# Kernel optimization log

Measured on AMD Instinct MI355X. Metric: run time of the kernel, lower is better.

## Reference

```python
import jax, jax.numpy as jnp
import numpy as np

N = 50000      # nodes
E = 800000     # edges (avg degree 16)
F = 6          # input node features
C = 64         # conv_hidden_channels
M = 256        # mlp_hidden_channels
NCLS = 24      # num_classes
EPS = 1e-5     # BatchNorm eps


def _bn(h, g, b):
    # BatchNorm1d in training mode: biased batch stats over the batch axis
    mu = h.mean(axis=0)
    var = ((h - mu) ** 2).mean(axis=0)
    return g * (h - mu) * jax.lax.rsqrt(var + EPS) + b


def _block(x, W, b, g, beta):
    # Lin -> ReLU -> BN  (one MLP block)
    return _bn(jax.nn.relu(x @ W + b), g, beta)


def _edge_conv(x, src, dst, Wa, ba, ga, bea, Wb, bb, gb, beb):
    # EdgeConv: message = MLP([x_i, x_j - x_i]), max-aggregated onto target i
    xi = x[dst]                                   # [E, d]
    xj = x[src]                                   # [E, d]
    e = jnp.concatenate([xi, xj - xi], axis=-1)   # [E, 2d]
    h = _block(_block(e, Wa, ba, ga, bea), Wb, bb, gb, beb)  # [E, C]
    agg = jax.ops.segment_max(h, dst, num_segments=N)        # [N, C]
    return jnp.where(jnp.isfinite(agg), agg, 0.0)  # zero-fill isolated nodes


def setup_inputs() -> dict:
    key = jax.random.key(0)
    ks = jax.random.split(key, 12)

    def w(k, shape, fan_in):
        return jax.random.normal(k, shape, jnp.float32) * (1.0 / np.sqrt(fan_in))

    z = lambda *s: jnp.zeros(s, jnp.float32)
    o = lambda *s: jnp.ones(s, jnp.float32)

    x = jax.random.normal(ks[0], (N, F), jnp.float32)
    edge_index = jax.random.randint(ks[1], (2, E), 0, N, jnp.int32)

    return {
        "x": x,
        # conv1 MLP: Lin(2F,C)+BN, Lin(C,C)+BN
        "W1a": w(ks[2], (2 * F, C), 2 * F), "b1a": z(C), "g1a": o(C), "be1a": z(C),
        "W1b": w(ks[3], (C, C), C),         "b1b": z(C), "g1b": o(C), "be1b": z(C),
        # conv2/conv3 stacked: Lin(2C,C)+BN, Lin(C,C)+BN
        "Wa": w(ks[4], (2, 2 * C, C), 2 * C), "ba": z(2, C), "ga": o(2, C), "bea": z(2, C),
        "Wb": w(ks[5], (2, C, C), C),         "bb": z(2, C), "gb": o(2, C), "beb": z(2, C),
        # lin1: Lin(3C, M)+BN
        "Wl": w(ks[6], (3 * C, M), 3 * C), "bl": z(M), "gl": o(M), "bel": z(M),
        # head: Lin(M, M/4)+BN, Lin(M/4, M/8)+BN, Lin(M/8, NCLS)
        "Wm1": w(ks[7], (M, M // 4), M),      "bm1": z(M // 4), "gm1": o(M // 4), "bem1": z(M // 4),
        "Wm2": w(ks[8], (M // 4, M // 8), M // 4), "bm2": z(M // 8), "gm2": o(M // 8), "bem2": z(M // 8),
        "Wo": w(ks[9], (M // 8, NCLS), M // 8), "bo": z(NCLS),
        "edge_index": edge_index,
    }


def reference(x, W1a, b1a, g1a, be1a, W1b, b1b, g1b, be1b,
              Wa, ba, ga, bea, Wb, bb, gb, beb,
              Wl, bl, gl, bel,
              Wm1, bm1, gm1, bem1, Wm2, bm2, gm2, bem2,
              Wo, bo, edge_index):
    src, dst = edge_index[0], edge_index[1]
    x1 = _edge_conv(x,  src, dst, W1a, b1a, g1a, be1a, W1b, b1b, g1b, be1b)
    x2 = _edge_conv(x1, src, dst, Wa[0], ba[0], ga[0], bea[0], Wb[0], bb[0], gb[0], beb[0])
    x3 = _edge_conv(x2, src, dst, Wa[1], ba[1], ga[1], bea[1], Wb[1], bb[1], gb[1], beb[1])
    h = _block(jnp.concatenate([x1, x2, x3], axis=-1), Wl, bl, gl, bel)
    h = _block(h, Wm1, bm1, gm1, bem1)   # Dropout is identity (eval)
    h = _block(h, Wm2, bm2, gm2, bem2)   # Dropout is identity (eval)
    logits = h @ Wo + bo
    return jax.nn.log_softmax(logits, axis=1)
```

## Files before the change

kernel.cpp:

```cpp
#include <hip/hip_runtime.h>
#include <hip/hip_bf16.h>

#define EPS 1e-5f
typedef unsigned short bfr;
typedef unsigned short hfr;
typedef _Float16 h2v __attribute__((ext_vector_type(2)));
typedef _Float16 f16x8 __attribute__((ext_vector_type(8)));
typedef float f32x4 __attribute__((ext_vector_type(4)));

#if defined(__has_builtin)
#if __has_builtin(__builtin_amdgcn_fdot2)
#define HAS_FDOT2 1
#endif
#endif

static inline int cdiv(int a, int b){ return (a + b - 1) / b; }
static inline int imin(int a, int b){ return a < b ? a : b; }

__device__ __forceinline__ float bf2f(bfr u){ return __uint_as_float((unsigned)u << 16); }
__device__ __forceinline__ bfr f2bf(float f){
  unsigned u = __float_as_uint(f);
  u += 0x7fffu + ((u >> 16) & 1u);
  return (bfr)(u >> 16);
}
__device__ __forceinline__ unsigned pack2bf(float a, float b){
  return (unsigned)f2bf(a) | ((unsigned)f2bf(b) << 16);
}
__device__ __forceinline__ float h2f(hfr u){ _Float16 h; __builtin_memcpy(&h, &u, 2); return (float)h; }
__device__ __forceinline__ hfr f2h(float f){ _Float16 h = (_Float16)f; hfr u; __builtin_memcpy(&u, &h, 2); return u; }
__device__ __forceinline__ unsigned pack2h(float a, float b){
  return (unsigned)f2h(a) | ((unsigned)f2h(b) << 16);
}
__device__ __forceinline__ h2v u2h2(unsigned u){ h2v r; __builtin_memcpy(&r, &u, 4); return r; }
__device__ __forceinline__ unsigned h22u(h2v h){ unsigned u; __builtin_memcpy(&u, &h, 4); return u; }
__device__ __forceinline__ float dot2(h2v a, h2v b, float c){
#ifdef HAS_FDOT2
  return __builtin_amdgcn_fdot2(a, b, c, false);
#else
  return c + (float)a.x * (float)b.x + (float)a.y * (float)b.y;
#endif
}

__global__ __launch_bounds__(256) void detect_kernel(const bfr* __restrict__ xr, int nwords, int* __restrict__ flag){
  int i = threadIdx.x;
  int bad = 0;
  if (i < nwords){
    bfr lo = xr[2 * i];
    int e = (lo >> 7) & 0xFF;
    bool plausible = ((lo & 0x7FFF) == 0) || (e >= 97 && e <= 157);
    bad = plausible ? 0 : 1;
  }
  __shared__ int s[256];
  s[threadIdx.x] = bad; __syncthreads();
  for (int st = 128; st; st >>= 1){
    if (threadIdx.x < st) s[threadIdx.x] += s[threadIdx.x + st];
    __syncthreads();
  }
  if (threadIdx.x == 0) *flag = (s[0] > 32) ? 1 : 0;
}

#define NPAR 31
struct ParamPtrs { const void* p[NPAR]; };
struct ParamOfs  { int off[NPAR + 1]; };

__global__ __launch_bounds__(256) void acvt_batch_kernel(ParamPtrs pp, ParamOfs po,
                                                         float* __restrict__ out, int total,
                                                         const int* __restrict__ flag){
  int g = blockIdx.x * 256 + threadIdx.x;
  if (g >= total) return;
  int isf = *flag;
  int t = 0;
  while (po.off[t + 1] <= g) ++t;
  int i = g - po.off[t];
  out[g] = isf ? ((const float*)pp.p[t])[i] : bf2f(((const bfr*)pp.p[t])[i]);
}

__global__ __launch_bounds__(256) void deg_kernel(const int* __restrict__ dst, int* __restrict__ deg, int E){
  int e = blockIdx.x * 256 + threadIdx.x;
  if (e < E) atomicAdd(&deg[dst[e]], 1);
}

__global__ __launch_bounds__(256) void scan1_kernel(const int* __restrict__ deg, int* __restrict__ locoff,
                                                    int* __restrict__ bsum, int N){
  __shared__ int s[256];
  int i = blockIdx.x * 256 + threadIdx.x;
  int v = (i < N) ? deg[i] : 0;
  s[threadIdx.x] = v; __syncthreads();
  for (int st = 1; st < 256; st <<= 1){
    int u = (threadIdx.x >= st) ? s[threadIdx.x - st] : 0;
    __syncthreads();
    s[threadIdx.x] += u;
    __syncthreads();
  }
  if (i < N) locoff[i] = s[threadIdx.x] - v;
  if (threadIdx.x == 255) bsum[blockIdx.x] = s[255];
}

__global__ __launch_bounds__(256) void scan2_kernel(int* __restrict__ bsum, int nb){
  __shared__ int s[256];
  const int t = threadIdx.x;
  int carry = 0;
  for (int base = 0; base < nb; base += 256){
    int v = (base + t < nb) ? bsum[base + t] : 0;
    s[t] = v; __syncthreads();
    for (int st = 1; st < 256; st <<= 1){
      int u = (t >= st) ? s[t - st] : 0;
      __syncthreads();
      s[t] += u;
      __syncthreads();
    }
    if (base + t < nb) bsum[base + t] = carry + s[t] - v;
    carry += s[255];
    __syncthreads();
  }
}

__global__ __launch_bounds__(256) void scan3_kernel(const int* __restrict__ locoff, const int* __restrict__ bsum,
                                                    int* __restrict__ row_off, int* __restrict__ cur,
                                                    int N, int E){
  int i = blockIdx.x * 256 + threadIdx.x;
  if (i < N){
    int v = locoff[i] + bsum[blockIdx.x];
    row_off[i] = v; cur[i] = v;
  }
  if (i == 0) row_off[N] = E;
}

__global__ __launch_bounds__(256) void scatter_kernel(const int* __restrict__ src, const int* __restrict__ dst,
                                                      int* __restrict__ cur, int* __restrict__ ssrc,
                                                      int* __restrict__ sdst, int E){
  int e = blockIdx.x * 256 + threadIdx.x;
  if (e < E){
    int d = dst[e];
    int p = atomicAdd(&cur[d], 1);
    ssrc[p] = src[e];
    sdst[p] = d;
  }
}

template<bool FIRST>
__global__ __launch_bounds__(256) void gemmPQ_kernel(const void* __restrict__ Av, int lda,
                                                     const float* __restrict__ Wa, int d,
                                                     const float* __restrict__ ba,
                                                     hfr* __restrict__ P, hfr* __restrict__ Q, int N){
  __shared__ unsigned WsU[64 * 64];
  const int y = blockIdx.y;
  const int tot = d * 64;
  if (FIRST){
    float* Ws = (float*)WsU;
    for (int i = threadIdx.x; i < tot; i += 256)
      Ws[i] = y ? Wa[tot + i] : (Wa[i] - Wa[tot + i]);
  } else {
    for (int i = threadIdx.x; i < 32 * 64; i += 256){
      int p = i >> 6, c = i & 63;
      int i0 = (2 * p) * 64 + c, i1 = (2 * p + 1) * 64 + c;
      float w0 = y ? Wa[tot + i0] : (Wa[i0] - Wa[tot + i0]);
      float w1 = y ? Wa[tot + i1] : (Wa[i1] - Wa[tot + i1]);
      WsU[i] = pack2h(w0, w1);
    }
  }
  __syncthreads();
  const int row = blockIdx.x * 256 + threadIdx.x;
  if (row >= N) return;
  float acc[64];
#pragma unroll
  for (int c = 0; c < 64; ++c) acc[c] = 0.f;
  if (FIRST){
    const float* Ws = (const float*)WsU;
    const float* Af = (const float*)Av + (size_t)row * lda;
    for (int k = 0; k < d; ++k){
      float a = Af[k];
      const float* wr = Ws + k * 64;
#pragma unroll
      for (int c4 = 0; c4 < 16; ++c4){
        float4 w = *(const float4*)(wr + 4 * c4);
        acc[4*c4+0] += a * w.x; acc[4*c4+1] += a * w.y;
        acc[4*c4+2] += a * w.z; acc[4*c4+3] += a * w.w;
      }
    }
  } else {
    const hfr* Ah = (const hfr*)Av + (size_t)row * lda;
#pragma unroll
    for (int k8 = 0; k8 < 8; ++k8){
      uint4 av = *(const uint4*)(Ah + k8 * 8);
      unsigned pr[4] = {av.x, av.y, av.z, av.w};
#pragma unroll
      for (int pi = 0; pi < 4; ++pi){
        h2v ap = u2h2(pr[pi]);
        const unsigned* wr = WsU + (k8 * 4 + pi) * 64;
#pragma unroll
        for (int c = 0; c < 64; ++c) acc[c] = dot2(ap, u2h2(wr[c]), acc[c]);
      }
    }
  }
  if (!y){
#pragma unroll
    for (int c = 0; c < 64; ++c) acc[c] += ba[c];
  }
  unsigned p[32];
#pragma unroll
  for (int c = 0; c < 64; c += 2) p[c / 2] = pack2h(acc[c], acc[c + 1]);
  hfr* outp = (y ? Q : P) + (size_t)row * 64;
  uint4* op = (uint4*)outp;
#pragma unroll
  for (int i = 0; i < 8; ++i) op[i] = make_uint4(p[4*i], p[4*i+1], p[4*i+2], p[4*i+3]);
}

template<int NOUT, int KSTEPS, bool FOLD>
__global__ __launch_bounds__(256) void mgemm_kernel(const hfr* __restrict__ Ah, int lda,
                                                    const float* __restrict__ Wp, const float* __restrict__ Wm, int ldw,
                                                    const float* __restrict__ bias,
                                                    const float* __restrict__ stats, float cntInv,
                                                    const float* __restrict__ g, const float* __restrict__ be,
                                                    hfr* __restrict__ Ov, int ldo,
                                                    int nrows, int relu){
  constexpr int K  = KSTEPS * 32;
  constexpr int KP = K + 8;
  constexpr int NT = NOUT / 16;
  __shared__ __align__(16) _Float16 W2T[NOUT * KP];
  __shared__ __align__(16) _Float16 etile[4][16][NOUT + 8];
  __shared__ float aS[FOLD ? K : 1], bbS[FOLD ? K : 1], bsum[FOLD ? 256 : 1];
  __shared__ float bfull[NOUT];
  const int tid = threadIdx.x;
  const int lane = tid & 63;
  const int wib = tid >> 6;
  const int colbase = blockIdx.y * NOUT;

  if (FOLD){
    for (int k = tid; k < K; k += 256){
      float mu = stats[k] * cntInv;
      float var = stats[K + k] * cntInv - mu * mu;
      float ai = g[k] * rsqrtf(var + EPS);
      aS[k] = ai; bbS[k] = be[k] - ai * mu;
    }
    __syncthreads();
  }
  for (int i = tid; i < K * NOUT; i += 256){
    int k = i / NOUT, c = i - k * NOUT;
    float w = Wp[(size_t)k * ldw + colbase + c];
    if (Wm) w -= Wm[(size_t)k * ldw + colbase + c];
    if (FOLD) w *= aS[k];
    W2T[c * KP + k] = (_Float16)w;
  }
  if (FOLD){
    constexpr int parts = 256 / NOUT;
    int c = tid % NOUT, p = tid / NOUT;
    float s = 0.f;
    for (int k = p; k < K; k += parts) s += bbS[k] * Wp[(size_t)k * ldw + colbase + c];
    bsum[p * NOUT + c] = s;
    __syncthreads();
    if (tid < NOUT){
      float t = bias[colbase + tid];
#pragma unroll
      for (int pp = 0; pp < parts; ++pp) t += bsum[pp * NOUT + tid];
      bfull[tid] = t;
    }
  } else {
    if (tid < NOUT) bfull[tid] = bias ? bias[colbase + tid] : 0.f;
  }
  __syncthreads();

  f16x8 Bf[KSTEPS][NT];
#pragma unroll
  for (int s = 0; s < KSTEPS; ++s)
#pragma unroll
    for (int t = 0; t < NT; ++t)
      Bf[s][t] = *(const f16x8*)&W2T[(t * 16 + (lane & 15)) * KP + s * 32 + (lane >> 4) * 8];
  float bc[NT];
#pragma unroll
  for (int t = 0; t < NT; ++t) bc[t] = bfull[t * 16 + (lane & 15)];

  const int ntiles = (nrows + 63) >> 6;
  for (int tile = blockIdx.x; tile < ntiles; tile += gridDim.x){
    const int r0 = tile * 64 + wib * 16;
    const int rowA = min(r0 + (lane & 15), nrows - 1);
    const hfr* Ap = Ah + (size_t)rowA * lda + (lane >> 4) * 8;
    f32x4 acc[NT];
#pragma unroll
    for (int t = 0; t < NT; ++t) acc[t] = (f32x4){bc[t], bc[t], bc[t], bc[t]};
#pragma unroll
    for (int s = 0; s < KSTEPS; ++s){
      f16x8 Af = *(const f16x8*)(Ap + s * 32);
#pragma unroll
      for (int t = 0; t < NT; ++t)
        acc[t] = __builtin_amdgcn_mfma_f32_16x16x32_f16(Af, Bf[s][t], acc[t], 0, 0, 0);
    }
#pragma unroll
    for (int t = 0; t < NT; ++t){
#pragma unroll
      for (int r = 0; r < 4; ++r){
        float v = acc[t][r];
        v = relu ? fmaxf(v, 0.f) : v;
        etile[wib][(lane >> 4) * 4 + r][t * 16 + (lane & 15)] = (_Float16)v;
      }
    }
    if (NOUT == 64){
#pragma unroll
      for (int h = 0; h < 2; ++h){
        int rl = h * 8 + (lane >> 3);
        int ch = lane & 7;
        uint4 vv = *(const uint4*)&etile[wib][rl][ch * 8];
        int rg = r0 + rl;
        if (rg < nrows) *(uint4*)(Ov + (size_t)rg * ldo + colbase + ch * 8) = vv;
      }
    } else {
      int rl = lane >> 2;
      int ch = lane & 3;
      uint4 vv = *(const uint4*)&etile[wib][rl][ch * 8];
      int rg = r0 + rl;
      if (rg < nrows) *(uint4*)(Ov + (size_t)rg * ldo + colbase + ch * 8) = vv;
    }
  }
}

__global__ __launch_bounds__(256) void passA_kernel(const hfr* __restrict__ P, const hfr* __restrict__ Q,
                                                    const int* __restrict__ ssrc, const int* __restrict__ sdst,
                                                    float* __restrict__ stats, int E){
  const int tid = threadIdx.x;
  const int lane = tid & 63;
  const int wib = tid >> 6;
  const int er0 = lane >> 3;
  const int ck = lane & 7;
  const int wid = (blockIdx.x * 256 + tid) >> 6;
  const int nw = (gridDim.x * 256) >> 6;
  const _Float16 z16 = (_Float16)0;
  const int lim = E - 1;
  float s8[8], q8[8];
#pragma unroll
  for (int j = 0; j < 8; ++j){ s8[j] = 0.f; q8[j] = 0.f; }
  for (int base = wid * 16; base < E; base += nw * 16){
    int idx = min(base + (lane & 15), lim);
    int sv = ssrc[idx];
    int dv = sdst[idx];
#pragma unroll
    for (int h = 0; h < 2; ++h){
      int er = h * 8 + er0;
      bool valid = (base + er) < E;
      int sj = __shfl(sv, er, 64);
      int dj = __shfl(dv, er, 64);
      uint4 qv = *((const uint4*)(Q + (size_t)sj * 64) + ck);
      uint4 pv = *((const uint4*)(P + (size_t)dj * 64) + ck);
      unsigned qa[4] = {qv.x, qv.y, qv.z, qv.w};
      unsigned pa[4] = {pv.x, pv.y, pv.z, pv.w};
#pragma unroll
      for (int t = 0; t < 4; ++t){
        h2v sm = u2h2(qa[t]) + u2h2(pa[t]);
        float v0 = (sm.x < z16) ? 0.f : (float)sm.x;
        float v1 = (sm.y < z16) ? 0.f : (float)sm.y;
        v0 = valid ? v0 : 0.f; v1 = valid ? v1 : 0.f;
        s8[2*t]   += v0; q8[2*t]   += v0 * v0;
        s8[2*t+1] += v1; q8[2*t+1] += v1 * v1;
      }
    }
  }
#pragma unroll
  for (int j = 0; j < 8; ++j){
    float s = s8[j], q = q8[j];
    s += __shfl_xor(s, 8, 64);  q += __shfl_xor(q, 8, 64);
    s += __shfl_xor(s, 16, 64); q += __shfl_xor(q, 16, 64);
    s += __shfl_xor(s, 32, 64); q += __shfl_xor(q, 32, 64);
    s8[j] = s; q8[j] = q;
  }
  __shared__ float ls[4][64], lq[4][64];
  if (lane < 8){
#pragma unroll
    for (int j = 0; j < 8; ++j){ ls[wib][lane * 8 + j] = s8[j]; lq[wib][lane * 8 + j] = q8[j]; }
  }
  __syncthreads();
  if (tid < 64){
    atomicAdd(&stats[tid], ls[0][tid] + ls[1][tid] + ls[2][tid] + ls[3][tid]);
  } else if (tid < 128){
    int c = tid - 64;
    atomicAdd(&stats[64 + c], lq[0][c] + lq[1][c] + lq[2][c] + lq[3][c]);
  }
}

__global__ __launch_bounds__(256) void passBC_kernel(const hfr* __restrict__ P, const hfr* __restrict__ Q,
                                                     const int* __restrict__ ssrc, const int* __restrict__ row_off,
                                                     const float* __restrict__ statsIn, float Einv,
                                                     const float* __restrict__ g1, const float* __restrict__ be1,
                                                     const float* __restrict__ Wb, const float* __restrict__ bn,
                                                     float* __restrict__ agg, float* __restrict__ statsOut, int N){
  __shared__ __align__(16) _Float16 W2T[64 * 72];
  __shared__ __align__(16) _Float16 ht[4][16][72];
  __shared__ float aS[64], bbS[64], b2S[64], bsum[256], qsum[256];
  const int tid = threadIdx.x;
  const int lane = tid & 63;
  const int er0 = lane >> 3;
  const int ck = lane & 7;
  const int wib = tid >> 6;
  const _Float16 z16 = (_Float16)0;
  if (tid < 64){
    float mu = statsIn[tid] * Einv;
    float var = statsIn[64 + tid] * Einv - mu * mu;
    float ai = g1[tid] * rsqrtf(var + EPS);
    aS[tid] = ai; bbS[tid] = be1[tid] - ai * mu;
  }
  __syncthreads();
  for (int i = tid; i < 4096; i += 256){
    int c = i >> 6, k = i & 63;
    W2T[c * 72 + k] = (_Float16)(aS[k] * Wb[(size_t)k * 64 + c]);
  }
  {
    int c = tid & 63, p = tid >> 6;
    float s = 0.f;
    for (int k = p; k < 64; k += 4) s += bbS[k] * Wb[(size_t)k * 64 + c];
    bsum[p * 64 + c] = s;
  }
  __syncthreads();
  if (tid < 64) b2S[tid] = bn[tid] + bsum[tid] + bsum[64 + tid] + bsum[128 + tid] + bsum[192 + tid];
  __syncthreads();
  f16x8 Bf[4][2];
#pragma unroll
  for (int t = 0; t < 4; ++t)
#pragma unroll
    for (int h = 0; h < 2; ++h){
      int c = t * 16 + (lane & 15);
      Bf[t][h] = *(const f16x8*)&W2T[c * 72 + h * 32 + (lane >> 4) * 8];
    }
  float bc[4];
#pragma unroll
  for (int t = 0; t < 4; ++t) bc[t] = b2S[t * 16 + (lane & 15)];
  _Float16 (*hl)[72] = ht[wib];
  const int wid = (blockIdx.x * 256 + tid) >> 6;
  const int nw = (gridDim.x * 256) >> 6;
  float sumT[4] = {0.f,0.f,0.f,0.f}, sqT[4] = {0.f,0.f,0.f,0.f};
  for (int n = wid; n < N; n += nw){
    const int e0 = row_off[n], e1 = row_off[n + 1];
    if (e0 >= e1) continue;
    uint4 pv4 = ((const uint4*)(P + (size_t)n * 64))[ck];
    h2v pp0 = u2h2(pv4.x), pp1 = u2h2(pv4.y), pp2 = u2h2(pv4.z), pp3 = u2h2(pv4.w);
    const int lim = e1 - 1;
    float mxT[4] = {0.f,0.f,0.f,0.f};
    for (int eb = e0; eb < e1; eb += 16){
      int sv = ssrc[min(eb + (lane & 15), lim)];
#pragma unroll
      for (int h = 0; h < 2; ++h){
        int er = h * 8 + er0;
        int sj = __shfl(sv, er, 64);
        uint4 qv = *((const uint4*)(Q + (size_t)sj * 64) + ck);
        h2v s0 = u2h2(qv.x) + pp0;
        h2v s1 = u2h2(qv.y) + pp1;
        h2v s2 = u2h2(qv.z) + pp2;
        h2v s3 = u2h2(qv.w) + pp3;
        s0.x = (s0.x < z16) ? z16 : s0.x; s0.y = (s0.y < z16) ? z16 : s0.y;
        s1.x = (s1.x < z16) ? z16 : s1.x; s1.y = (s1.y < z16) ? z16 : s1.y;
        s2.x = (s2.x < z16) ? z16 : s2.x; s2.y = (s2.y < z16) ? z16 : s2.y;
        s3.x = (s3.x < z16) ? z16 : s3.x; s3.y = (s3.y < z16) ? z16 : s3.y;
        *(uint4*)&hl[er][ck * 8] = make_uint4(h22u(s0), h22u(s1), h22u(s2), h22u(s3));
      }
      f16x8 A0 = *(const f16x8*)&hl[lane & 15][(lane >> 4) * 8];
      f16x8 A1 = *(const f16x8*)&hl[lane & 15][32 + (lane >> 4) * 8];
#pragma unroll
      for (int t = 0; t < 4; ++t){
        f32x4 Cv = {bc[t], bc[t], bc[t], bc[t]};
        Cv = __builtin_amdgcn_mfma_f32_16x16x32_f16(A0, Bf[t][0], Cv, 0, 0, 0);
        Cv = __builtin_amdgcn_mfma_f32_16x16x32_f16(A1, Bf[t][1], Cv, 0, 0, 0);
#pragma unroll
        for (int r = 0; r < 4; ++r){
          float v = fmaxf(Cv[r], 0.f);
          int rowi = (lane >> 4) * 4 + r;
          bool valid = (eb + rowi) < e1;
          mxT[t] = fmaxf(mxT[t], v);
          sumT[t] += valid ? v : 0.f;
          sqT[t]  += valid ? v * v : 0.f;
        }
      }
    }
#pragma unroll
    for (int t = 0; t < 4; ++t){
      float m = mxT[t];
      m = fmaxf(m, __shfl_xor(m, 16, 64));
      m = fmaxf(m, __shfl_xor(m, 32, 64));
      mxT[t] = m;
    }
    float outv = (lane < 16) ? mxT[0] : (lane < 32) ? mxT[1] : (lane < 48) ? mxT[2] : mxT[3];
    agg[(size_t)n * 64 + lane] = outv;
  }
#pragma unroll
  for (int t = 0; t < 4; ++t){
    float s = sumT[t], q = sqT[t];
    s += __shfl_xor(s, 16, 64); s += __shfl_xor(s, 32, 64);
    q += __shfl_xor(q, 16, 64); q += __shfl_xor(q, 32, 64);
    sumT[t] = s; sqT[t] = q;
  }
  float ssel = (lane < 16) ? sumT[0] : (lane < 32) ? sumT[1] : (lane < 48) ? sumT[2] : sumT[3];
  float qsel = (lane < 16) ? sqT[0]  : (lane < 32) ? sqT[1]  : (lane < 48) ? sqT[2]  : sqT[3];
  bsum[tid] = ssel; qsum[tid] = qsel;
  __syncthreads();
  if (tid < 64){
    atomicAdd(&statsOut[tid], bsum[tid] + bsum[64 + tid] + bsum[128 + tid] + bsum[192 + tid]);
  } else if (tid < 128){
    int c = tid - 64;
    atomicAdd(&statsOut[64 + c], qsum[c] + qsum[64 + c] + qsum[128 + c] + qsum[192 + c]);
  }
}

__global__ __launch_bounds__(256) void fixup_kernel(const float* __restrict__ agg, const int* __restrict__ deg,
                                                    const float* __restrict__ stats, float cntInv,
                                                    const float* __restrict__ g, const float* __restrict__ be,
                                                    hfr* __restrict__ xout, int ldx, int N){
  int t = blockIdx.x * 256 + threadIdx.x;
  if (t >= N * 64) return;
  int n = t >> 6, c = t & 63;
  float mu = stats[c] * cntInv;
  float var = stats[64 + c] * cntInv - mu * mu;
  float a = g[c] * rsqrtf(var + EPS);
  float b = be[c] - a * mu;
  float v = 0.f;
  if (deg[n] > 0) v = a * agg[t] + b;
  xout[(size_t)n * ldx + c] = f2h(v);
}

template<int C>
__global__ __launch_bounds__(256) void statsN_kernel(const hfr* __restrict__ u, float* __restrict__ stats, int N){
  constexpr int RP = 256 / C;
  const int c = threadIdx.x % C, j = threadIdx.x / C;
  float sum = 0.f, sq = 0.f;
  for (int r = blockIdx.x * RP + j; r < N; r += gridDim.x * RP){
    float v = h2f(u[(size_t)r * C + c]);
    sum += v; sq += v * v;
  }
  __shared__ float ls[256], lq[256];
  ls[threadIdx.x] = sum; lq[threadIdx.x] = sq;
  __syncthreads();
  if (threadIdx.x < C){
    float s = 0.f, q = 0.f;
#pragma unroll
    for (int jj = 0; jj < RP; ++jj){ s += ls[jj * C + c]; q += lq[jj * C + c]; }
    atomicAdd(&stats[c], s); atomicAdd(&stats[C + c], q);
  }
}

__global__ __launch_bounds__(256) void head_kernel(const hfr* __restrict__ u2,
                                                   const float* __restrict__ stats, float cntInv,
                                                   const float* __restrict__ g, const float* __restrict__ be,
                                                   const float* __restrict__ Wo, const float* __restrict__ bo,
                                                   void* __restrict__ out, int N, const int* __restrict__ flag){
  __shared__ float Ws[32 * 24];
  __shared__ float bs[24];
  __shared__ float aS[32], bbS[32];
  const int tid = threadIdx.x;
  if (tid < 32){
    float mu = stats[tid] * cntInv;
    float var = stats[32 + tid] * cntInv - mu * mu;
    float ai = g[tid] * rsqrtf(var + EPS);
    aS[tid] = ai; bbS[tid] = be[tid] - ai * mu;
  }
  __syncthreads();
  for (int i = tid; i < 32 * 24; i += 256){
    int k = i / 24, c = i - 24 * k;
    Ws[i] = aS[k] * Wo[(size_t)k * 24 + c];
  }
  if (tid < 24){
    float t = bo[tid];
    for (int k = 0; k < 32; ++k) t += bbS[k] * Wo[(size_t)k * 24 + tid];
    bs[tid] = t;
  }
  __syncthreads();
  int r = blockIdx.x * 256 + tid;
  if (r >= N) return;
  int isf = *flag;
  float l[24];
#pragma unroll
  for (int c = 0; c < 24; ++c) l[c] = bs[c];
  const hfr* up = u2 + (size_t)r * 32;
#pragma unroll
  for (int k = 0; k < 32; ++k){
    float v = h2f(up[k]);
#pragma unroll
    for (int c = 0; c < 24; ++c) l[c] += v * Ws[k * 24 + c];
  }
  float m = l[0];
#pragma unroll
  for (int c = 1; c < 24; ++c) m = fmaxf(m, l[c]);
  float s = 0.f;
#pragma unroll
  for (int c = 0; c < 24; ++c) s += expf(l[c] - m);
  float lse = m + logf(s);
  if (isf){
    float4* op = (float4*)((float*)out + (size_t)r * 24);
#pragma unroll
    for (int i = 0; i < 6; ++i)
      op[i] = make_float4(l[4*i] - lse, l[4*i+1] - lse, l[4*i+2] - lse, l[4*i+3] - lse);
  } else {
    unsigned p[12];
#pragma unroll
    for (int c = 0; c < 24; c += 2) p[c / 2] = pack2bf(l[c] - lse, l[c + 1] - lse);
    uint4* op = (uint4*)((bfr*)out + (size_t)r * 24);
#pragma unroll
    for (int i = 0; i < 3; ++i) op[i] = make_uint4(p[4*i], p[4*i+1], p[4*i+2], p[4*i+3]);
  }
}

extern "C" void kernel_launch(void* const* d_in, const int* in_sizes, int n_in,
                              void* d_out, int out_size, void* d_ws, size_t ws_size,
                              hipStream_t stream){
  const int N = in_sizes[0] / 6;
  const int E = in_sizes[31] / 2;
  const int* edge = (const int*)d_in[31];
  const int* src = edge;
  const int* dst = edge + E;

  size_t off = 0; char* basep = (char*)d_ws;
  auto alloc = [&](size_t bytes) -> void* {
    void* p = basep + off;
    off = (off + bytes + 255) & ~(size_t)255;
    return p;
  };
  float* stA  = (float*)alloc(1472 * 4);
  float* stN1 = stA + 768;
  float* stN2 = stA + 1280;
  float* stN3 = stA + 1408;
  int*   flag = (int*)  alloc(4);
  int*   deg  = (int*)  alloc((size_t)N * 4);
  int*   rowo = (int*)  alloc((size_t)(N + 1) * 4);
  int*   cur  = (int*)  alloc((size_t)N * 4);
  int*   loco = (int*)  alloc((size_t)N * 4);
  int*   bsc  = (int*)  alloc(1024 * 4);
  int*   ssrc = (int*)  alloc((size_t)E * 4);
  int*   sdst = (int*)  alloc((size_t)E * 4);

  ParamPtrs pp; ParamOfs po;
  int hoff[32]; int total = 0;
  for (int s = 0; s < NPAR; ++s){
    int idx = (s < 30) ? (s + 1) : 0;
    pp.p[s] = d_in[idx];
    po.off[s] = total;
    hoff[idx] = total;
    total += in_sizes[idx];
  }
  po.off[NPAR] = total;
  float* pf = (float*)alloc((size_t)total * 4);

  hfr*   P    = (hfr*)  alloc((size_t)N * 64 * 2);
  hfr*   Qb   = (hfr*)  alloc((size_t)N * 64 * 2);
  float* agg  = (float*)alloc((size_t)N * 64 * 4);
  hfr*   xcat = (hfr*)  alloc((size_t)N * 192 * 2);
  hfr* u_l = (hfr*)P;
  hfr* u1  = xcat;
  hfr* u2  = xcat + (size_t)N * 64;
  (void)ws_size; (void)n_in; (void)out_size;

  dim3 B(256);
  detect_kernel<<<1, B, 0, stream>>>((const bfr*)d_in[0], 256, flag);
  acvt_batch_kernel<<<cdiv(total, 256), B, 0, stream>>>(pp, po, pf, total, flag);

  hipMemsetAsync(stA, 0, 1472 * 4, stream);
  hipMemsetAsync(deg, 0, (size_t)N * 4, stream);
  deg_kernel<<<cdiv(E, 256), B, 0, stream>>>(dst, deg, E);
  const int NBn = cdiv(N, 256);
  scan1_kernel<<<NBn, B, 0, stream>>>(deg, loco, bsc, N);
  scan2_kernel<<<1, B, 0, stream>>>(bsc, NBn);
  scan3_kernel<<<NBn, B, 0, stream>>>(loco, bsc, rowo, cur, N, E);
  scatter_kernel<<<cdiv(E, 256), B, 0, stream>>>(src, dst, cur, ssrc, sdst, E);

  const int NB = cdiv(N, 256);
  const int ntiles = cdiv(N, 64);
  const int GWA = 1024, GWB = 1024;
  const float Einv = 1.f / (float)E;
  for (int k = 0; k < 3; ++k){
    const float *Wa_k, *ba_k, *ga_k, *bea_k, *Wb_k, *bb_k, *gb_k, *beb_k;
    if (k == 0){
      Wa_k = pf + hoff[1]; ba_k = pf + hoff[2]; ga_k = pf + hoff[3]; bea_k = pf + hoff[4];
      Wb_k = pf + hoff[5]; bb_k = pf + hoff[6]; gb_k = pf + hoff[7]; beb_k = pf + hoff[8];
    } else {
      int kk = k - 1;
      Wa_k = pf + hoff[9]  + (size_t)kk * 128 * 64;
      ba_k = pf + hoff[10] + kk * 64;
      ga_k = pf + hoff[11] + kk * 64;
      bea_k= pf + hoff[12] + kk * 64;
      Wb_k = pf + hoff[13] + (size_t)kk * 64 * 64;
      bb_k = pf + hoff[14] + kk * 64;
      gb_k = pf + hoff[15] + kk * 64;
      beb_k= pf + hoff[16] + kk * 64;
    }
    float* st1 = stA + k * 256;
    float* st2 = st1 + 128;
    if (k == 0){
      gemmPQ_kernel<true><<<dim3(NB, 2), B, 0, stream>>>(pf + hoff[0], 6, Wa_k, 6, ba_k, P, Qb, N);
    } else {
      mgemm_kernel<64, 2, false><<<dim3(imin(ntiles, 1024), 1), B, 0, stream>>>(
          xcat + (size_t)(k - 1) * 64, 192, Wa_k, Wa_k + 64 * 64, 64, ba_k,
          nullptr, 0.f, nullptr, nullptr, P, 64, N, 0);
      mgemm_kernel<64, 2, false><<<dim3(imin(ntiles, 1024), 1), B, 0, stream>>>(
          xcat + (size_t)(k - 1) * 64, 192, Wa_k + 64 * 64, nullptr, 64, nullptr,
          nullptr, 0.f, nullptr, nullptr, Qb, 64, N, 0);
    }
    passA_kernel<<<GWA, B, 0, stream>>>(P, Qb, ssrc, sdst, st1, E);
    passBC_kernel<<<GWB, B, 0, stream>>>(P, Qb, ssrc, rowo, st1, Einv, ga_k, bea_k, Wb_k, bb_k,
                                         agg, st2, N);
    fixup_kernel<<<cdiv(N * 64, 256), B, 0, stream>>>(agg, deg, st2, Einv, gb_k, beb_k,
                                                      xcat + (size_t)k * 64, 192, N);
  }

  mgemm_kernel<64, 6, false><<<dim3(imin(ntiles, 256), 4), B, 0, stream>>>(
      xcat, 192, pf + hoff[17], nullptr, 256, pf + hoff[18],
      nullptr, 0.f, nullptr, nullptr, u_l, 256, N, 1);
  statsN_kernel<256><<<512, B, 0, stream>>>(u_l, stN1, N);
  mgemm_kernel<32, 8, true><<<dim3(imin(ntiles, 512), 2), B, 0, stream>>>(
      u_l, 256, pf + hoff[21], nullptr, 64, pf + hoff[22],
      stN1, 1.f / (float)N, pf + hoff[19], pf + hoff[20], u1, 64, N, 1);
  statsN_kernel<64><<<512, B, 0, stream>>>(u1, stN2, N);
  mgemm_kernel<32, 2, true><<<dim3(imin(ntiles, 1024), 1), B, 0, stream>>>(
      u1, 64, pf + hoff[25], nullptr, 32, pf + hoff[26],
      stN2, 1.f / (float)N, pf + hoff[23], pf + hoff[24], u2, 32, N, 1);
  statsN_kernel<32><<<512, B, 0, stream>>>(u2, stN3, N);
  head_kernel<<<cdiv(N, 256), B, 0, stream>>>(u2, stN3, 1.f / (float)N, pf + hoff[27], pf + hoff[28],
                                              pf + hoff[29], pf + hoff[30], d_out, N, flag);
  (void)NB;
}
```

Before: 775.4 us.

## Materialize first-layer edge activations once and reuse them in the MFMA pass

passA now walks the CSR by destination node, computes relu(P[dst]+Q[src]) once, writes it to a new E×64 fp16 buffer h1 and accumulates BN stats from it. passBC then reads h1 contiguously instead of regathering P and Q. This removes the sdst array and the second gather of Q, at the cost of writing and reading about 100MB of edge activations per layer. It also merges the P and Q GEMMs into one launch and vectorizes statsN to 16-byte loads.

Measured after the change: 745.8 us. -3.8%, faster.

```diff
diff --git a/kernel.cpp b/kernel.cpp
--- a/kernel.cpp
+++ b/kernel.cpp
@@ -127,14 +127,12 @@
 }
 
 __global__ __launch_bounds__(256) void scatter_kernel(const int* __restrict__ src, const int* __restrict__ dst,
-                                                      int* __restrict__ cur, int* __restrict__ ssrc,
-                                                      int* __restrict__ sdst, int E){
+                                                      int* __restrict__ cur, int* __restrict__ ssrc, int E){
   int e = blockIdx.x * 256 + threadIdx.x;
   if (e < E){
     int d = dst[e];
     int p = atomicAdd(&cur[d], 1);
     ssrc[p] = src[e];
-    sdst[p] = d;
   }
 }
 
@@ -206,13 +204,13 @@
   for (int i = 0; i < 8; ++i) op[i] = make_uint4(p[4*i], p[4*i+1], p[4*i+2], p[4*i+3]);
 }
 
-template<int NOUT, int KSTEPS, bool FOLD>
+template<int NOUT, int KSTEPS, bool FOLD, bool PQ>
 __global__ __launch_bounds__(256) void mgemm_kernel(const hfr* __restrict__ Ah, int lda,
-                                                    const float* __restrict__ Wp, const float* __restrict__ Wm, int ldw,
-                                                    const float* __restrict__ bias,
+                                                    const float* __restrict__ Wp0, const float* __restrict__ Wm0, int ldw,
+                                                    const float* __restrict__ bias0,
                                                     const float* __restrict__ stats, float cntInv,
                                                     const float* __restrict__ g, const float* __restrict__ be,
-                                                    hfr* __restrict__ Ov, int ldo,
+                                                    hfr* __restrict__ Ov0, hfr* __restrict__ Ov1, int ldo,
                                                     int nrows, int relu){
   constexpr int K  = KSTEPS * 32;
   constexpr int KP = K + 8;
@@ -224,7 +222,16 @@
   const int tid = threadIdx.x;
   const int lane = tid & 63;
   const int wib = tid >> 6;
-  const int colbase = blockIdx.y * NOUT;
+  const float* Wp = Wp0;
+  const float* Wm = Wm0;
+  const float* bias = bias0;
+  hfr* Ov = Ov0;
+  int colbase = blockIdx.y * NOUT;
+  if (PQ){
+    colbase = 0;
+    if (blockIdx.y == 1){ Wp = Wp0 + (size_t)K * ldw; Wm = nullptr; bias = nullptr; Ov = Ov1; }
+    else { Wm = Wp0 + (size_t)K * ldw; }
+  }
 
   if (FOLD){
     for (int k = tid; k < K; k += 256){
@@ -314,8 +321,8 @@
 }
 
 __global__ __launch_bounds__(256) void passA_kernel(const hfr* __restrict__ P, const hfr* __restrict__ Q,
-                                                    const int* __restrict__ ssrc, const int* __restrict__ sdst,
-                                                    float* __restrict__ stats, int E){
+                                                    const int* __restrict__ ssrc, const int* __restrict__ row_off,
+                                                    float* __restrict__ stats, hfr* __restrict__ h1, int N){
   const int tid = threadIdx.x;
   const int lane = tid & 63;
   const int wib = tid >> 6;
@@ -324,119 +331,21 @@
   const int wid = (blockIdx.x * 256 + tid) >> 6;
   const int nw = (gridDim.x * 256) >> 6;
   const _Float16 z16 = (_Float16)0;
-  const int lim = E - 1;
   float s8[8], q8[8];
 #pragma unroll
   for (int j = 0; j < 8; ++j){ s8[j] = 0.f; q8[j] = 0.f; }
-  for (int base = wid * 16; base < E; base += nw * 16){
-    int idx = min(base + (lane & 15), lim);
-    int sv = ssrc[idx];
-    int dv = sdst[idx];
-#pragma unroll
-    for (int h = 0; h < 2; ++h){
-      int er = h * 8 + er0;
-      bool valid = (base + er) < E;
-      int sj = __shfl(sv, er, 64);
-      int dj = __shfl(dv, er, 64);
-      uint4 qv = *((const uint4*)(Q + (size_t)sj * 64) + ck);
-      uint4 pv = *((const uint4*)(P + (size_t)dj * 64) + ck);
-      unsigned qa[4] = {qv.x, qv.y, qv.z, qv.w};
-      unsigned pa[4] = {pv.x, pv.y, pv.z, pv.w};
-#pragma unroll
-      for (int t = 0; t < 4; ++t){
-        h2v sm = u2h2(qa[t]) + u2h2(pa[t]);
-        float v0 = (sm.x < z16) ? 0.f : (float)sm.x;
-        float v1 = (sm.y < z16) ? 0.f : (float)sm.y;
-        v0 = valid ? v0 : 0.f; v1 = valid ? v1 : 0.f;
-        s8[2*t]   += v0; q8[2*t]   += v0 * v0;
-        s8[2*t+1] += v1; q8[2*t+1] += v1 * v1;
-      }
-    }
-  }
-#pragma unroll
-  for (int j = 0; j < 8; ++j){
-    float s = s8[j], q = q8[j];
-    s += __shfl_xor(s, 8, 64);  q += __shfl_xor(q, 8, 64);
-    s += __shfl_xor(s, 16, 64); q += __shfl_xor(q, 16, 64);
-    s += __shfl_xor(s, 32, 64); q += __shfl_xor(q, 32, 64);
-    s8[j] = s; q8[j] = q;
-  }
-  __shared__ float ls[4][64], lq[4][64];
-  if (lane < 8){
-#pragma unroll
-    for (int j = 0; j < 8; ++j){ ls[wib][lane * 8 + j] = s8[j]; lq[wib][lane * 8 + j] = q8[j]; }
-  }
-  __syncthreads();
-  if (tid < 64){
-    atomicAdd(&stats[tid], ls[0][tid] + ls[1][tid] + ls[2][tid] + ls[3][tid]);
-  } else if (tid < 128){
-    int c = tid - 64;
-    atomicAdd(&stats[64 + c], lq[0][c] + lq[1][c] + lq[2][c] + lq[3][c]);
-  }
-}
-
-__global__ __launch_bounds__(256) void passBC_kernel(const hfr* __restrict__ P, const hfr* __restrict__ Q,
-                                                     const int* __restrict__ ssrc, const int* __restrict__ row_off,
-                                                     const float* __restrict__ statsIn, float Einv,
-                                                     const float* __restrict__ g1, const float* __restrict__ be1,
-                                                     const float* __restrict__ Wb, const float* __restrict__ bn,
-                                                     float* __restrict__ agg, float* __restrict__ statsOut, int N){
-  __shared__ __align__(16) _Float16 W2T[64 * 72];
-  __shared__ __align__(16) _Float16 ht[4][16][72];
-  __shared__ float aS[64], bbS[64], b2S[64], bsum[256], qsum[256];
-  const int tid = threadIdx.x;
-  const int lane = tid & 63;
-  const int er0 = lane >> 3;
-  const int ck = lane & 7;
-  const int wib = tid >> 6;
-  const _Float16 z16 = (_Float16)0;
-  if (tid < 64){
-    float mu = statsIn[tid] * Einv;
-    float var = statsIn[64 + tid] * Einv - mu * mu;
-    float ai = g1[tid] * rsqrtf(var + EPS);
-    aS[tid] = ai; bbS[tid] = be1[tid] - ai * mu;
-  }
-  __syncthreads();
-  for (int i = tid; i < 4096; i += 256){
-    int c = i >> 6, k = i & 63;
-    W2T[c * 72 + k] = (_Float16)(aS[k] * Wb[(size_t)k * 64 + c]);
-  }
-  {
-    int c = tid & 63, p = tid >> 6;
-    float s = 0.f;
-    for (int k = p; k < 64; k += 4) s += bbS[k] * Wb[(size_t)k * 64 + c];
-    bsum[p * 64 + c] = s;
-  }
-  __syncthreads();
-  if (tid < 64) b2S[tid] = bn[tid] + bsum[tid] + bsum[64 + tid] + bsum[128 + tid] + bsum[192 + tid];
-  __syncthreads();
-  f16x8 Bf[4][2];
-#pragma unroll
-  for (int t = 0; t < 4; ++t)
-#pragma unroll
-    for (int h = 0; h < 2; ++h){
-      int c = t * 16 + (lane & 15);
-      Bf[t][h] = *(const f16x8*)&W2T[c * 72 + h * 32 + (lane >> 4) * 8];
-    }
-  float bc[4];
-#pragma unroll
-  for (int t = 0; t < 4; ++t) bc[t] = b2S[t * 16 + (lane & 15)];
-  _Float16 (*hl)[72] = ht[wib];
-  const int wid = (blockIdx.x * 256 + tid) >> 6;
-  const int nw = (gridDim.x * 256) >> 6;
-  float sumT[4] = {0.f,0.f,0.f,0.f}, sqT[4] = {0.f,0.f,0.f,0.f};
   for (int n = wid; n < N; n += nw){
     const int e0 = row_off[n], e1 = row_off[n + 1];
     if (e0 >= e1) continue;
     uint4 pv4 = ((const uint4*)(P + (size_t)n * 64))[ck];
     h2v pp0 = u2h2(pv4.x), pp1 = u2h2(pv4.y), pp2 = u2h2(pv4.z), pp3 = u2h2(pv4.w);
     const int lim = e1 - 1;
-    float mxT[4] = {0.f,0.f,0.f,0.f};
     for (int eb = e0; eb < e1; eb += 16){
       int sv = ssrc[min(eb + (lane & 15), lim)];
 #pragma unroll
       for (int h = 0; h < 2; ++h){
         int er = h * 8 + er0;
+        int ge = eb + er;
         int sj = __shfl(sv, er, 64);
         uint4 qv = *((const uint4*)(Q + (size_t)sj * 64) + ck);
         h2v s0 = u2h2(qv.x) + pp0;
@@ -447,10 +356,95 @@
         s1.x = (s1.x < z16) ? z16 : s1.x; s1.y = (s1.y < z16) ? z16 : s1.y;
         s2.x = (s2.x < z16) ? z16 : s2.x; s2.y = (s2.y < z16) ? z16 : s2.y;
         s3.x = (s3.x < z16) ? z16 : s3.x; s3.y = (s3.y < z16) ? z16 : s3.y;
-        *(uint4*)&hl[er][ck * 8] = make_uint4(h22u(s0), h22u(s1), h22u(s2), h22u(s3));
+        if (ge < e1){
+          *(uint4*)(h1 + (size_t)ge * 64 + ck * 8) = make_uint4(h22u(s0), h22u(s1), h22u(s2), h22u(s3));
+          float v;
+          v = (float)s0.x; s8[0] += v; q8[0] = fmaf(v, v, q8[0]);
+          v = (float)s0.y; s8[1] += v; q8[1] = fmaf(v, v, q8[1]);
+          v = (float)s1.x; s8[2] += v; q8[2] = fmaf(v, v, q8[2]);
+          v = (float)s1.y; s8[3] += v; q8[3] = fmaf(v, v, q8[3]);
+          v = (float)s2.x; s8[4] += v; q8[4] = fmaf(v, v, q8[4]);
+          v = (float)s2.y; s8[5] += v; q8[5] = fmaf(v, v, q8[5]);
+          v = (float)s3.x; s8[6] += v; q8[6] = fmaf(v, v, q8[6]);
+          v = (float)s3.y; s8[7] += v; q8[7] = fmaf(v, v, q8[7]);
+        }
       }
-      f16x8 A0 = *(const f16x8*)&hl[lane & 15][(lane >> 4) * 8];
-      f16x8 A1 = *(const f16x8*)&hl[lane & 15][32 + (lane >> 4) * 8];
+    }
+  }
+#pragma unroll
+  for (int j = 0; j < 8; ++j){
+    float s = s8[j], q = q8[j];
+    s += __shfl_xor(s, 8, 64);  q += __shfl_xor(q, 8, 64);
+    s += __shfl_xor(s, 16, 64); q += __shfl_xor(q, 16, 64);
+    s += __shfl_xor(s, 32, 64); q += __shfl_xor(q, 32, 64);
+    s8[j] = s; q8[j] = q;
+  }
+  __shared__ float ls[4][64], lq[4][64];
+  if (lane < 8){
+#pragma unroll
+    for (int j = 0; j < 8; ++j){ ls[wib][lane * 8 + j] = s8[j]; lq[wib][lane * 8 + j] = q8[j]; }
+  }
+  __syncthreads();
+  if (tid < 64){
+    atomicAdd(&stats[tid], ls[0][tid] + ls[1][tid] + ls[2][tid] + ls[3][tid]);
+  } else if (tid < 128){
+    int c = tid - 64;
+    atomicAdd(&stats[64 + c], lq[0][c] + lq[1][c] + lq[2][c] + lq[3][c]);
+  }
+}
+
+__global__ __launch_bounds__(256) void passBC_kernel(const hfr* __restrict__ h1,
+                                                     const int* __restrict__ row_off,
+                                                     const float* __restrict__ statsIn, float Einv,
+                                                     const float* __restrict__ g1, const float* __restrict__ be1,
+                                                     const float* __restrict__ Wb, const float* __restrict__ bn,
+                                                     float* __restrict__ agg, float* __restrict__ statsOut, int N){
+  __shared__ __align__(16) _Float16 W2T[64 * 72];
+  __shared__ float aS[64], bbS[64], b2S[64], bsum[256], qsum[256];
+  const int tid = threadIdx.x;
+  const int lane = tid & 63;
+  if (tid < 64){
+    float mu = statsIn[tid] * Einv;
+    float var = statsIn[64 + tid] * Einv - mu * mu;
+    float ai = g1[tid] * rsqrtf(var + EPS);
+    aS[tid] = ai; bbS[tid] = be1[tid] - ai * mu;
+  }
+  __syncthreads();
+  for (int i = tid; i < 4096; i += 256){
+    int c = i >> 6, k = i & 63;
+    W2T[c * 72 + k] = (_Float16)(aS[k] * Wb[(size_t)k * 64 + c]);
+  }
+  {
+    int c = tid & 63, p = tid >> 6;
+    float s = 0.f;
+    for (int k = p; k < 64; k += 4) s += bbS[k] * Wb[(size_t)k * 64 + c];
+    bsum[p * 64 + c] = s;
+  }
+  __syncthreads();
+  if (tid < 64) b2S[tid] = bn[tid] + bsum[tid] + bsum[64 + tid] + bsum[128 + tid] + bsum[192 + tid];
+  __syncthreads();
+  f16x8 Bf[4][2];
+#pragma unroll
+  for (int t = 0; t < 4; ++t)
+#pragma unroll
+    for (int h = 0; h < 2; ++h){
+      int c = t * 16 + (lane & 15);
+      Bf[t][h] = *(const f16x8*)&W2T[c * 72 + h * 32 + (lane >> 4) * 8];
+    }
+  float bc[4];
+#pragma unroll
+  for (int t = 0; t < 4; ++t) bc[t] = b2S[t * 16 + (lane & 15)];
+  const int wid = (blockIdx.x * 256 + tid) >> 6;
+  const int nw = (gridDim.x * 256) >> 6;
+  float sumT[4] = {0.f,0.f,0.f,0.f}, sqT[4] = {0.f,0.f,0.f,0.f};
+  for (int n = wid; n < N; n += nw){
+    const int e0 = row_off[n], e1 = row_off[n + 1];
+    if (e0 >= e1) continue;
+    float mxT[4] = {0.f,0.f,0.f,0.f};
+    for (int eb = e0; eb < e1; eb += 16){
+      const hfr* ap = h1 + (size_t)(eb + (lane & 15)) * 64 + (lane >> 4) * 8;
+      f16x8 A0 = *(const f16x8*)ap;
+      f16x8 A1 = *(const f16x8*)(ap + 32);
 #pragma unroll
       for (int t = 0; t < 4; ++t){
         f32x4 Cv = {bc[t], bc[t], bc[t], bc[t]};
@@ -458,12 +452,12 @@
         Cv = __builtin_amdgcn_mfma_f32_16x16x32_f16(A1, Bf[t][1], Cv, 0, 0, 0);
 #pragma unroll
         for (int r = 0; r < 4; ++r){
+          int rowi = (lane >> 4) * 4 + r;
           float v = fmaxf(Cv[r], 0.f);
-          int rowi = (lane >> 4) * 4 + r;
-          bool valid = (eb + rowi) < e1;
+          v = ((eb + rowi) < e1) ? v : 0.f;
           mxT[t] = fmaxf(mxT[t], v);
-          sumT[t] += valid ? v : 0.f;
-          sqT[t]  += valid ? v * v : 0.f;
+          sumT[t] += v;
+          sqT[t]  = fmaf(v, v, sqT[t]);
         }
       }
     }
@@ -514,21 +508,33 @@
 
 template<int C>
 __global__ __launch_bounds__(256) void statsN_kernel(const hfr* __restrict__ u, float* __restrict__ stats, int N){
-  constexpr int RP = 256 / C;
-  const int c = threadIdx.x % C, j = threadIdx.x / C;
-  float sum = 0.f, sq = 0.f;
-  for (int r = blockIdx.x * RP + j; r < N; r += gridDim.x * RP){
-    float v = h2f(u[(size_t)r * C + c]);
-    sum += v; sq += v * v;
-  }
-  __shared__ float ls[256], lq[256];
-  ls[threadIdx.x] = sum; lq[threadIdx.x] = sq;
+  constexpr int CH = C / 8;
+  constexpr int RP = 256 / CH;
+  const int ch = threadIdx.x % CH;
+  const int j0 = threadIdx.x / CH;
+  float s[8], q[8];
+#pragma unroll
+  for (int j = 0; j < 8; ++j){ s[j] = 0.f; q[j] = 0.f; }
+  for (int r = blockIdx.x * RP + j0; r < N; r += gridDim.x * RP){
+    uint4 v = *(const uint4*)(u + (size_t)r * C + ch * 8);
+    unsigned w[4] = {v.x, v.y, v.z, v.w};
+#pragma unroll
+    for (int t = 0; t < 4; ++t){
+      h2v p = u2h2(w[t]);
+      float a = (float)p.x, b = (float)p.y;
+      s[2*t]   += a; q[2*t]   = fmaf(a, a, q[2*t]);
+      s[2*t+1] += b; q[2*t+1] = fmaf(b, b, q[2*t+1]);
+    }
+  }
+  __shared__ float ls[256][9], lq[256][9];
+#pragma unroll
+  for (int j = 0; j < 8; ++j){ ls[threadIdx.x][j] = s[j]; lq[threadIdx.x][j] = q[j]; }
   __syncthreads();
   if (threadIdx.x < C){
-    float s = 0.f, q = 0.f;
-#pragma unroll
-    for (int jj = 0; jj < RP; ++jj){ s += ls[jj * C + c]; q += lq[jj * C + c]; }
-    atomicAdd(&stats[c], s); atomicAdd(&stats[C + c], q);
+    int c = threadIdx.x, ch2 = c >> 3, jj = c & 7;
+    float ss = 0.f, qq = 0.f;
+    for (int p = 0; p < RP; ++p){ ss += ls[p * CH + ch2][jj]; qq += lq[p * CH + ch2][jj]; }
+    atomicAdd(&stats[c], ss); atomicAdd(&stats[C + c], qq);
   }
 }
 
@@ -619,7 +625,6 @@
   int*   loco = (int*)  alloc((size_t)N * 4);
   int*   bsc  = (int*)  alloc(1024 * 4);
   int*   ssrc = (int*)  alloc((size_t)E * 4);
-  int*   sdst = (int*)  alloc((size_t)E * 4);
 
   ParamPtrs pp; ParamOfs po;
   int hoff[32]; int total = 0;
@@ -637,6 +642,7 @@
   hfr*   Qb   = (hfr*)  alloc((size_t)N * 64 * 2);
   float* agg  = (float*)alloc((size_t)N * 64 * 4);
   hfr*   xcat = (hfr*)  alloc((size_t)N * 192 * 2);
+  hfr*   h1   = (hfr*)  alloc((size_t)(E + 16) * 64 * 2);
   hfr* u_l = (hfr*)P;
   hfr* u1  = xcat;
   hfr* u2  = xcat + (size_t)N * 64;
@@ -648,12 +654,13 @@
 
   hipMemsetAsync(stA, 0, 1472 * 4, stream);
   hipMemsetAsync(deg, 0, (size_t)N * 4, stream);
+  hipMemsetAsync(h1 + (size_t)E * 64, 0, 16 * 64 * 2, stream);
   deg_kernel<<<cdiv(E, 256), B, 0, stream>>>(dst, deg, E);
   const int NBn = cdiv(N, 256);
   scan1_kernel<<<NBn, B, 0, stream>>>(deg, loco, bsc, N);
   scan2_kernel<<<1, B, 0, stream>>>(bsc, NBn);
   scan3_kernel<<<NBn, B, 0, stream>>>(loco, bsc, rowo, cur, N, E);
-  scatter_kernel<<<cdiv(E, 256), B, 0, stream>>>(src, dst, cur, ssrc, sdst, E);
+  scatter_kernel<<<cdiv(E, 256), B, 0, stream>>>(src, dst, cur, ssrc, E);
 
   const int NB = cdiv(N, 256);
   const int ntiles = cdiv(N, 64);
@@ -680,31 +687,28 @@
     if (k == 0){
       gemmPQ_kernel<true><<<dim3(NB, 2), B, 0, stream>>>(pf + hoff[0], 6, Wa_k, 6, ba_k, P, Qb, N);
     } else {
-      mgemm_kernel<64, 2, false><<<dim3(imin(ntiles, 1024), 1), B, 0, stream>>>(
-          xcat + (size_t)(k - 1) * 64, 192, Wa_k, Wa_k + 64 * 64, 64, ba_k,
-          nullptr, 0.f, nullptr, nullptr, P, 64, N, 0);
-      mgemm_kernel<64, 2, false><<<dim3(imin(ntiles, 1024), 1), B, 0, stream>>>(
-          xcat + (size_t)(k - 1) * 64, 192, Wa_k + 64 * 64, nullptr, 64, nullptr,
-          nullptr, 0.f, nullptr, nullptr, Qb, 64, N, 0);
-    }
-    passA_kernel<<<GWA, B, 0, stream>>>(P, Qb, ssrc, sdst, st1, E);
-    passBC_kernel<<<GWB, B, 0, stream>>>(P, Qb, ssrc, rowo, st1, Einv, ga_k, bea_k, Wb_k, bb_k,
+      mgemm_kernel<64, 2, false, true><<<dim3(imin(ntiles, 1024), 2), B, 0, stream>>>(
+          xcat + (size_t)(k - 1) * 64, 192, Wa_k, nullptr, 64, ba_k,
+          nullptr, 0.f, nullptr, nullptr, P, Qb, 64, N, 0);
+    }
+    passA_kernel<<<GWA, B, 0, stream>>>(P, Qb, ssrc, rowo, st1, h1, N);
+    passBC_kernel<<<GWB, B, 0, stream>>>(h1, rowo, st1, Einv, ga_k, bea_k, Wb_k, bb_k,
                                          agg, st2, N);
     fixup_kernel<<<cdiv(N * 64, 256), B, 0, stream>>>(agg, deg, st2, Einv, gb_k, beb_k,
                                                       xcat + (size_t)k * 64, 192, N);
   }
 
-  mgemm_kernel<64, 6, false><<<dim3(imin(ntiles, 256), 4), B, 0, stream>>>(
+  mgemm_kernel<64, 6, false, false><<<dim3(imin(ntiles, 256), 4), B, 0, stream>>>(
       xcat, 192, pf + hoff[17], nullptr, 256, pf + hoff[18],
-      nullptr, 0.f, nullptr, nullptr, u_l, 256, N, 1);
+      nullptr, 0.f, nullptr, nullptr, u_l, nullptr, 256, N, 1);
   statsN_kernel<256><<<512, B, 0, stream>>>(u_l, stN1, N);
-  mgemm_kernel<32, 8, true><<<dim3(imin(ntiles, 512), 2), B, 0, stream>>>(
+  mgemm_kernel<32, 8, true, false><<<dim3(imin(ntiles, 512), 2), B, 0, stream>>>(
       u_l, 256, pf + hoff[21], nullptr, 64, pf + hoff[22],
-      stN1, 1.f / (float)N, pf + hoff[19], pf + hoff[20], u1, 64, N, 1);
+      stN1, 1.f / (float)N, pf + hoff[19], pf + hoff[20], u1, nullptr, 64, N, 1);
   statsN_kernel<64><<<512, B, 0, stream>>>(u1, stN2, N);
-  mgemm_kernel<32, 2, true><<<dim3(imin(ntiles, 1024), 1), B, 0, stream>>>(
+  mgemm_kernel<32, 2, true, false><<<dim3(imin(ntiles, 1024), 1), B, 0, stream>>>(
       u1, 64, pf + hoff[25], nullptr, 32, pf + hoff[26],
-      stN2, 1.f / (float)N, pf + hoff[23], pf + hoff[24], u2, 32, N, 1);
+      stN2, 1.f / (float)N, pf + hoff[23], pf + hoff[24], u2, nullptr, 32, N, 1);
   statsN_kernel<32><<<512, B, 0, stream>>>(u2, stN3, N);
   head_kernel<<<cdiv(N, 256), B, 0, stream>>>(u2, stN3, 1.f / (float)N, pf + hoff[27], pf + hoff[28],
                                               pf + hoff[29], pf + hoff[30], d_out, N, flag);
```
